# Kernel tuning notes

Hardware: AMD Instinct MI355X
Metric: run time of the kernel (lower is better)

## Reference

```python
import jax, jax.numpy as jnp
import numpy as np

N_VAR = 2048   # number of variable nodes
DEG = 4        # edges per variable node
N_EDGE = N_VAR * DEG  # 8192 expanded/duplicated edge messages
BATCH = 32
DENSITY = 8.0 / N_EDGE  # sparse Tanner-style edge-edge connectivity


def setup_inputs() -> dict:
    key = jax.random.key(0)
    k1, k2, k3 = jax.random.split(key, 3)
    inp = jax.random.normal(k1, (BATCH, N_EDGE), dtype=jnp.float32)
    llr = jax.random.normal(k2, (BATCH, N_VAR), dtype=jnp.float32)
    # binary sparse mask [E_out, E_in]
    mask = (jax.random.uniform(k3, (N_EDGE, N_EDGE)) < DENSITY).astype(jnp.float32)
    # llr_expander: one-hot rows mapping each edge to its variable node [E, N_VAR]
    var_idx = jnp.tile(jnp.arange(N_VAR), DEG)
    llr_expander = jax.nn.one_hot(var_idx, N_VAR, dtype=jnp.float32)
    # learned params, initialized as in the module (ones, pre-masked)
    input_weight = mask * jnp.ones((N_EDGE, N_EDGE), dtype=jnp.float32)
    llr_weight = jnp.ones((1, N_VAR), dtype=jnp.float32)
    return {"input": inp, "input_weight": input_weight, "mask": mask,
            "llr": llr, "llr_weight": llr_weight, "llr_expander": llr_expander}


def reference(input, input_weight, mask, llr, llr_weight, llr_expander):
    # x = 0.5 * ( expand(w_llr * llr) + input @ (mask * W).T )
    weighted_input = input @ (mask * input_weight).T          # [B, E]
    expanded_llr = (llr_weight * llr) @ llr_expander.T        # [B, E]
    return 0.5 * (expanded_llr + weighted_input)
```

## Files before the change

### kernel.cpp

```cpp
#include <hip/hip_runtime.h>


#define N_VAR  2048
#define N_EDGE 8192
#define BATCH  32
#define BLOCK  256
#define CAP    32

typedef unsigned int u32x4 __attribute__((ext_vector_type(4)));

__global__ __launch_bounds__(BLOCK) void bp_scan(
    const float* __restrict__ mask,
    unsigned*    __restrict__ cnt,
    unsigned*    __restrict__ cols)
{
    const int wave = threadIdx.x >> 6;
    const int lane = threadIdx.x & 63;
    const int row  = blockIdx.x * (BLOCK / 64) + wave;

    const u32x4* __restrict__ mrow = (const u32x4*)(mask + (size_t)row * N_EDGE);
    unsigned* __restrict__ rcols = cols + (size_t)row * CAP;

    const unsigned long long lt_mask = (1ull << lane) - 1ull;
    unsigned total = 0;

    u32x4 buf[32];
    #pragma unroll
    for (int r = 0; r < 32; ++r)
        buf[r] = mrow[r * 64 + lane];

    #pragma unroll
    for (int r = 0; r < 32; ++r) {
        const u32x4 v = buf[r];
        if (__ballot((v.x | v.y | v.z | v.w) != 0u)) {
            const unsigned c[4] = { v.x, v.y, v.z, v.w };
            const int colbase = (r * 64 + lane) * 4;
            #pragma unroll
            for (int j = 0; j < 4; ++j) {
                const bool hit = (c[j] != 0u);
                const unsigned long long bal = __ballot(hit);
                if (bal) {
                    if (hit) {
                        const unsigned idx =
                            total + (unsigned)__popcll(bal & lt_mask);
                        if (idx < CAP)
                            rcols[idx] = (unsigned)(colbase + j);
                    }
                    total += (unsigned)__popcll(bal);
                }
            }
        }
    }

    if (lane == 0) cnt[row] = (total < CAP) ? total : CAP;
}

__global__ __launch_bounds__(BLOCK) void bp_acc(
    const float* __restrict__ input,
    const float* __restrict__ weight,
    const float* __restrict__ llr,
    const float* __restrict__ llr_w,
    const unsigned* __restrict__ cnt,
    const unsigned* __restrict__ cols,
    float* __restrict__ out)
{
    const int wave = threadIdx.x >> 6;
    const int lane = threadIdx.x & 63;
    const int row  = blockIdx.x * (BLOCK / 64) + wave;
    const int b    = lane & (BATCH - 1);

    const int n = (int)cnt[row];
    int   c = 0;
    float w = 0.0f;
    if (lane < n) {
        c = (int)cols[(size_t)row * CAP + lane];
        w = weight[(size_t)row * N_EDGE + c];
    }

    float acc = 0.0f;
    for (int i = 0; i < n; ++i) {
        const float wb = __shfl(w, i);
        const int   cb = __shfl(c, i);
        acc = fmaf(wb, input[(size_t)b * N_EDGE + cb], acc);
    }

    if (lane < BATCH) {
        const int v = row & (N_VAR - 1);
        const float llr_term = llr_w[v] * llr[(size_t)b * N_VAR + v];
        out[(size_t)b * N_EDGE + row] = 0.5f * (acc + llr_term);
    }
}

extern "C" void kernel_launch(void* const* d_in, const int* in_sizes, int n_in,
                              void* d_out, int out_size, void* d_ws, size_t ws_size,
                              hipStream_t stream) {
    const float* input  = (const float*)d_in[0];
    const float* weight = (const float*)d_in[1];
    const float* mask   = (const float*)d_in[2];
    const float* llr    = (const float*)d_in[3];
    const float* llr_w  = (const float*)d_in[4];
    float* out = (float*)d_out;

    unsigned* cnt  = (unsigned*)d_ws;
    unsigned* cols = (unsigned*)((char*)d_ws + N_EDGE * 4);

    const int grid = N_EDGE / (BLOCK / 64);
    bp_scan<<<grid, BLOCK, 0, stream>>>(mask, cnt, cols);
    bp_acc <<<grid, BLOCK, 0, stream>>>(input, weight, llr, llr_w, cnt, cols, out);
}
```

Baseline: 500.8 us.

## Stream mask rows through LDS with double-buffered async global-to-LDS loads

The mask scan no longer loads a whole 32 KB row into 32 vector registers per lane. Each wave now double-buffers 512-float chunks into LDS with global_load_lds and waits on a manual vmcnt so the next chunk's load overlaps scanning of the current one. This cuts register pressure and should allow more waves in flight on a scan that is bound by memory bandwidth. The trade-off is fewer bytes outstanding per wave, plus hand-encoded waitcnt values that are fragile. A redundant min on cnt is also added in the accumulate kernel.

```diff
diff --git a/kernel.cpp b/kernel.cpp
--- a/kernel.cpp
+++ b/kernel.cpp
@@ -6,6 +6,8 @@
 #define BATCH  32
 #define BLOCK  256
 #define CAP    32
+#define CHUNK  512
+#define NCHUNK (N_EDGE / CHUNK)
 
 typedef unsigned int u32x4 __attribute__((ext_vector_type(4)));
 
@@ -14,39 +16,67 @@
     unsigned*    __restrict__ cnt,
     unsigned*    __restrict__ cols)
 {
+    __shared__ __align__(16) float lbuf[4][2][CHUNK];
+
     const int wave = threadIdx.x >> 6;
     const int lane = threadIdx.x & 63;
     const int row  = blockIdx.x * (BLOCK / 64) + wave;
 
-    const u32x4* __restrict__ mrow = (const u32x4*)(mask + (size_t)row * N_EDGE);
+    const float* __restrict__ mrow = mask + (size_t)row * N_EDGE;
     unsigned* __restrict__ rcols = cols + (size_t)row * CAP;
 
     const unsigned long long lt_mask = (1ull << lane) - 1ull;
     unsigned total = 0;
 
-    u32x4 buf[32];
     #pragma unroll
-    for (int r = 0; r < 32; ++r)
-        buf[r] = mrow[r * 64 + lane];
+    for (int i = 0; i < 2; ++i)
+        __builtin_amdgcn_global_load_lds(
+            (const __attribute__((address_space(1))) void*)
+                (mrow + i * 256 + lane * 4),
+            (__attribute__((address_space(3))) void*)&lbuf[wave][0][i * 256],
+            16, 0, 0);
 
     #pragma unroll
-    for (int r = 0; r < 32; ++r) {
-        const u32x4 v = buf[r];
-        if (__ballot((v.x | v.y | v.z | v.w) != 0u)) {
-            const unsigned c[4] = { v.x, v.y, v.z, v.w };
-            const int colbase = (r * 64 + lane) * 4;
+    for (int c = 0; c < NCHUNK; ++c) {
+        const int cur = c & 1;
+        if (c + 1 < NCHUNK) {
             #pragma unroll
-            for (int j = 0; j < 4; ++j) {
-                const bool hit = (c[j] != 0u);
-                const unsigned long long bal = __ballot(hit);
-                if (bal) {
-                    if (hit) {
-                        const unsigned idx =
-                            total + (unsigned)__popcll(bal & lt_mask);
-                        if (idx < CAP)
-                            rcols[idx] = (unsigned)(colbase + j);
+            for (int i = 0; i < 2; ++i)
+                __builtin_amdgcn_global_load_lds(
+                    (const __attribute__((address_space(1))) void*)
+                        (mrow + (c + 1) * CHUNK + i * 256 + lane * 4),
+                    (__attribute__((address_space(3))) void*)
+                        &lbuf[wave][cur ^ 1][i * 256],
+                    16, 0, 0);
+        }
+        __builtin_amdgcn_sched_barrier(0);
+        if (c + 1 < NCHUNK)
+            __builtin_amdgcn_s_waitcnt(0x0F72);
+        else
+            __builtin_amdgcn_s_waitcnt(0x0F70);
+        __builtin_amdgcn_sched_barrier(0);
+
+        #pragma unroll
+        for (int i = 0; i < 2; ++i) {
+            const u32x4 v =
+                *(const u32x4*)&lbuf[wave][cur][i * 256 + lane * 4];
+            if (__ballot((v.x | v.y | v.z | v.w) != 0u)) {
+                const unsigned cc[4] = { v.x, v.y, v.z, v.w };
+                const unsigned colbase =
+                    (unsigned)(c * CHUNK + i * 256 + lane * 4);
+                #pragma unroll
+                for (int j = 0; j < 4; ++j) {
+                    const bool hit = (cc[j] != 0u);
+                    const unsigned long long bal = __ballot(hit);
+                    if (bal) {
+                        if (hit) {
+                            const unsigned idx =
+                                total + (unsigned)__popcll(bal & lt_mask);
+                            if (idx < CAP)
+                                rcols[idx] = colbase + (unsigned)j;
+                        }
+                        total += (unsigned)__popcll(bal);
                     }
-                    total += (unsigned)__popcll(bal);
                 }
             }
         }
@@ -69,7 +99,7 @@
     const int row  = blockIdx.x * (BLOCK / 64) + wave;
     const int b    = lane & (BATCH - 1);
 
-    const int n = (int)cnt[row];
+    const int n = min((int)cnt[row], CAP);
     int   c = 0;
     float w = 0.0f;
     if (lane < n) {
```

New measurement: 501.7 us. No clear change (+0.2%).
